# Performance work log

Measured on AMD Instinct MI355X. Metric: run time of the kernel, lower is better.

The kernel has to match this reference:

```python
import jax, jax.numpy as jnp
import numpy as np

M = 8192          # flattened tokens (batch*seq)
IN_FEATURES = 4096
OUT_FEATURES = 4096


def setup_inputs() -> dict:
    key = jax.random.key(0)
    k1, k2, k3 = jax.random.split(key, 3)
    # int8-valued activations and weights, stored as int32 (values in [-128, 127])
    x = jax.random.randint(k1, (M, IN_FEATURES), -128, 128, dtype=jnp.int32)
    int_weight = jax.random.randint(k2, (OUT_FEATURES, IN_FEATURES), -128, 127, dtype=jnp.int32)
    bias = (jax.random.normal(k3, (OUT_FEATURES,), dtype=jnp.float32) * 0.02).astype(jnp.float16)
    return {"x": x, "int_weight": int_weight, "bias": bias}


def reference(x, int_weight, bias):
    # x.to(torch.int8); quik int8Matmul: int8 GEMM with int32 accumulation, out = x @ W^T
    x_i8 = x.astype(jnp.int8)
    w_i8 = int_weight.astype(jnp.int8)
    acc = jax.lax.dot_general(
        x_i8, w_i8,
        dimension_numbers=(((1,), (1,)), ((), ())),  # [M, K] x [N, K] -> [M, N]
        preferred_element_type=jnp.int32,
    )
    # .to(torch.float16) then bias add (fused epilogue target)
    return acc.astype(jnp.float16) + bias
```

## Files before the change

kernel.cpp:

```cpp
#include <hip/hip_runtime.h>

#define MDIM 8192
#define NDIM 4096
#define KDIM 4096
#define BM 256
#define BN 128
#define BK 128

typedef int v4i __attribute__((ext_vector_type(4)));
typedef int v16i __attribute__((ext_vector_type(16)));

__device__ __forceinline__ unsigned pack4(int x, int y, int z, int w) {
    return (unsigned)(x & 0xff) | ((unsigned)(y & 0xff) << 8) |
           ((unsigned)(z & 0xff) << 16) | ((unsigned)w << 24);
}

__global__ __launch_bounds__(256) void pack_tiled(const int* __restrict__ x,
                                                  const int* __restrict__ w,
                                                  uint4* __restrict__ xp,
                                                  uint4* __restrict__ wp) {
    __shared__ unsigned lds32[256 * 33];
    const int wg  = blockIdx.x;
    const int tid = threadIdx.x;
    const int kq   = tid & 31;
    const int rsub = tid >> 5;

    if (wg < 1024) {
        const int mtile = wg >> 5, kiter = wg & 31;
        const int* base = x + (size_t)(mtile * 256) * KDIM + kiter * 128;
#pragma unroll
        for (int it = 0; it < 32; ++it) {
            const int row = it * 8 + rsub;
            int4 v = *(const int4*)(base + (size_t)row * KDIM + kq * 4);
            lds32[row * 33 + kq] = pack4(v.x, v.y, v.z, v.w);
        }
        __syncthreads();
        uint4* dst = xp + (size_t)(mtile * 32 + kiter) * 8192;
#pragma unroll
        for (int it = 0; it < 8; ++it) {
            const int g = it * 256 + tid;
            const int kb = g >> 8, row = g & 255;
            const unsigned* p = &lds32[row * 33 + kb * 4];
            uint4 o;
            o.x = p[0]; o.y = p[1]; o.z = p[2]; o.w = p[3];
            dst[g] = o;
        }
    } else {
        const int ntile = (wg - 1024) >> 5, kiter = wg & 31;
        const int* base = w + (size_t)(ntile * 128) * KDIM + kiter * 128;
#pragma unroll
        for (int it = 0; it < 16; ++it) {
            const int row = it * 8 + rsub;
            int4 v = *(const int4*)(base + (size_t)row * KDIM + kq * 4);
            lds32[row * 33 + kq] = pack4(v.x, v.y, v.z, v.w);
        }
        __syncthreads();
        uint4* dst = wp + (size_t)(ntile * 32 + kiter) * 4096;
#pragma unroll
        for (int it = 0; it < 16; ++it) {
            const int g = it * 256 + tid;
            const int kb = g >> 7, row = g & 127;
            const unsigned* p = &lds32[row * 33 + kb * 4];
            uint4 o;
            o.x = p[0]; o.y = p[1]; o.z = p[2]; o.w = p[3];
            dst[g] = o;
        }
    }
}

template <bool PACKED>
__global__ __launch_bounds__(256, 2) void gemm_i8(const char* __restrict__ Ap,
                                                  const char* __restrict__ Bp,
                                                  const int* __restrict__ A32,
                                                  const int* __restrict__ B32,
                                                  const _Float16* __restrict__ bias,
                                                  _Float16* __restrict__ out) {
    __shared__ char lds[49152];

    const int tid  = threadIdx.x;
    const int lane = tid & 63;
    const int wave = tid >> 6;
    const int bm0 = blockIdx.y * BM;
    const int bn0 = blockIdx.x * BN;

    const char* apan = Ap + (size_t)blockIdx.y * (BM * KDIM) + lane * 16;
    const char* bpan = Bp + (size_t)blockIdx.x * (BN * KDIM) + lane * 16;

    int aoffs[8], boffs[4];
    if constexpr (!PACKED) {
#pragma unroll
        for (int r = 0; r < 8; ++r) {
            const int c = r * 4 + wave;
            aoffs[r] = (bm0 + (c & 3) * 64 + lane) * KDIM + (c >> 2) * 16;
        }
#pragma unroll
        for (int r = 0; r < 4; ++r) {
            const int c = r * 4 + wave;
            boffs[r] = (bn0 + (c & 1) * 64 + lane) * KDIM + (c >> 1) * 16;
        }
    }

    const int wr  = wave >> 1;
    const int wc  = wave & 1;
    const int l31 = lane & 31;
    const int kg  = lane >> 5;
    int abase[4], bbase[2];
#pragma unroll
    for (int mt = 0; mt < 4; ++mt)
        abase[mt] = kg * 4096 + (wr * 128 + mt * 32 + l31) * 16;
#pragma unroll
    for (int nt = 0; nt < 2; ++nt)
        bbase[nt] = 32768 + kg * 2048 + (wc * 64 + nt * 32 + l31) * 16;

    v16i acc[4][2];
#pragma unroll
    for (int mt = 0; mt < 4; ++mt)
#pragma unroll
        for (int nt = 0; nt < 2; ++nt)
#pragma unroll
            for (int i = 0; i < 16; ++i) acc[mt][nt][i] = 0;

    for (int k0 = 0; k0 < KDIM; k0 += BK) {
        if constexpr (PACKED) {
#pragma unroll
            for (int r = 0; r < 8; ++r) {
                const int c = r * 4 + wave;
                __builtin_amdgcn_global_load_lds(
                    (__attribute__((address_space(1))) void*)(apan + c * 1024),
                    (__attribute__((address_space(3))) void*)(lds + c * 1024), 16, 0, 0);
            }
#pragma unroll
            for (int r = 0; r < 4; ++r) {
                const int c = r * 4 + wave;
                __builtin_amdgcn_global_load_lds(
                    (__attribute__((address_space(1))) void*)(bpan + c * 1024),
                    (__attribute__((address_space(3))) void*)(lds + 32768 + c * 1024), 16, 0, 0);
            }
            apan += BM * BK;
            bpan += BN * BK;
        } else {
#pragma unroll
            for (int r = 0; r < 8; ++r) {
                const int c = r * 4 + wave;
                const int4* s = (const int4*)(A32 + (size_t)aoffs[r]);
                int4 v0 = s[0], v1 = s[1], v2 = s[2], v3 = s[3];
                uint4 pk;
                pk.x = pack4(v0.x, v0.y, v0.z, v0.w);
                pk.y = pack4(v1.x, v1.y, v1.z, v1.w);
                pk.z = pack4(v2.x, v2.y, v2.z, v2.w);
                pk.w = pack4(v3.x, v3.y, v3.z, v3.w);
                *(uint4*)(lds + c * 1024 + lane * 16) = pk;
                aoffs[r] += BK;
            }
#pragma unroll
            for (int r = 0; r < 4; ++r) {
                const int c = r * 4 + wave;
                const int4* s = (const int4*)(B32 + (size_t)boffs[r]);
                int4 v0 = s[0], v1 = s[1], v2 = s[2], v3 = s[3];
                uint4 pk;
                pk.x = pack4(v0.x, v0.y, v0.z, v0.w);
                pk.y = pack4(v1.x, v1.y, v1.z, v1.w);
                pk.z = pack4(v2.x, v2.y, v2.z, v2.w);
                pk.w = pack4(v3.x, v3.y, v3.z, v3.w);
                *(uint4*)(lds + 32768 + c * 1024 + lane * 16) = pk;
                boffs[r] += BK;
            }
        }
        __syncthreads();

#pragma unroll
        for (int ks = 0; ks < 4; ++ks) {
            v4i af[4], bf[2];
#pragma unroll
            for (int mt = 0; mt < 4; ++mt)
                af[mt] = *(const v4i*)(lds + abase[mt] + ks * 8192);
#pragma unroll
            for (int nt = 0; nt < 2; ++nt)
                bf[nt] = *(const v4i*)(lds + bbase[nt] + ks * 4096);
#pragma unroll
            for (int mt = 0; mt < 4; ++mt)
#pragma unroll
                for (int nt = 0; nt < 2; ++nt)
                    acc[mt][nt] = __builtin_amdgcn_mfma_i32_32x32x32_i8(
                        af[mt], bf[nt], acc[mt][nt], 0, 0, 0);
        }

        __syncthreads();
    }

    const _Float16 bv0 = bias[bn0 + wc * 64 + l31];
    const _Float16 bv1 = bias[bn0 + wc * 64 + 32 + l31];
#pragma unroll
    for (int mt = 0; mt < 4; ++mt) {
#pragma unroll
        for (int nt = 0; nt < 2; ++nt) {
            const int gcol = bn0 + wc * 64 + nt * 32 + l31;
            const _Float16 bb = nt ? bv1 : bv0;
#pragma unroll
            for (int r = 0; r < 16; ++r) {
                const int rit  = (r & 3) + 8 * (r >> 2) + 4 * kg;
                const int grow = bm0 + wr * 128 + mt * 32 + rit;
                _Float16 h = (_Float16)(float)acc[mt][nt][r] + bb;
                out[(size_t)grow * NDIM + gcol] = h;
            }
        }
    }
}

extern "C" void kernel_launch(void* const* d_in, const int* in_sizes, int n_in,
                              void* d_out, int out_size, void* d_ws, size_t ws_size,
                              hipStream_t stream) {
    const int* x = (const int*)d_in[0];
    const int* w = (const int*)d_in[1];
    const _Float16* bias = (const _Float16*)d_in[2];
    _Float16* out = (_Float16*)d_out;

    const size_t xbytes = (size_t)MDIM * KDIM;
    const size_t wbytes = (size_t)NDIM * KDIM;

    if (ws_size >= xbytes + wbytes) {
        char* xp = (char*)d_ws;
        char* wp = xp + xbytes;
        pack_tiled<<<2048, 256, 0, stream>>>(x, w, (uint4*)xp, (uint4*)wp);
        gemm_i8<true><<<dim3(NDIM / BN, MDIM / BM), 256, 0, stream>>>(
            xp, wp, nullptr, nullptr, bias, out);
    } else {
        gemm_i8<false><<<dim3(NDIM / BN, MDIM / BM), 256, 0, stream>>>(
            nullptr, nullptr, x, w, bias, out);
    }
}
```

Measured before the change: 411.8 us.

## Load packed B fragments straight into registers and fix packed tile strides

Result: faster. 396.8 us (-3.6%).

```diff
diff --git a/kernel.cpp b/kernel.cpp
--- a/kernel.cpp
+++ b/kernel.cpp
@@ -35,7 +35,7 @@
             lds32[row * 33 + kq] = pack4(v.x, v.y, v.z, v.w);
         }
         __syncthreads();
-        uint4* dst = xp + (size_t)(mtile * 32 + kiter) * 8192;
+        uint4* dst = xp + (size_t)(mtile * 32 + kiter) * 2048;
 #pragma unroll
         for (int it = 0; it < 8; ++it) {
             const int g = it * 256 + tid;
@@ -55,11 +55,14 @@
             lds32[row * 33 + kq] = pack4(v.x, v.y, v.z, v.w);
         }
         __syncthreads();
-        uint4* dst = wp + (size_t)(ntile * 32 + kiter) * 4096;
-#pragma unroll
-        for (int it = 0; it < 16; ++it) {
-            const int g = it * 256 + tid;
-            const int kb = g >> 7, row = g & 127;
+        uint4* dst = wp + (size_t)(ntile * 32 + kiter) * 1024;
+#pragma unroll
+        for (int it = 0; it < 4; ++it) {
+            const int g  = it * 256 + tid;
+            const int ln = g & 63, h = g >> 6;
+            const int wc2 = h >> 3, nt = (h >> 2) & 1, ks = h & 3;
+            const int row = wc2 * 64 + nt * 32 + (ln & 31);
+            const int kb  = 2 * ks + (ln >> 5);
             const unsigned* p = &lds32[row * 33 + kb * 4];
             uint4 o;
             o.x = p[0]; o.y = p[1]; o.z = p[2]; o.w = p[3];
@@ -75,42 +78,34 @@
                                                   const int* __restrict__ B32,
                                                   const _Float16* __restrict__ bias,
                                                   _Float16* __restrict__ out) {
-    __shared__ char lds[49152];
+    __shared__ char lds[32768];
 
     const int tid  = threadIdx.x;
     const int lane = tid & 63;
     const int wave = tid >> 6;
     const int bm0 = blockIdx.y * BM;
     const int bn0 = blockIdx.x * BN;
-
-    const char* apan = Ap + (size_t)blockIdx.y * (BM * KDIM) + lane * 16;
-    const char* bpan = Bp + (size_t)blockIdx.x * (BN * KDIM) + lane * 16;
-
-    int aoffs[8], boffs[4];
-    if constexpr (!PACKED) {
-#pragma unroll
-        for (int r = 0; r < 8; ++r) {
-            const int c = r * 4 + wave;
-            aoffs[r] = (bm0 + (c & 3) * 64 + lane) * KDIM + (c >> 2) * 16;
-        }
-#pragma unroll
-        for (int r = 0; r < 4; ++r) {
-            const int c = r * 4 + wave;
-            boffs[r] = (bn0 + (c & 1) * 64 + lane) * KDIM + (c >> 1) * 16;
-        }
-    }
-
     const int wr  = wave >> 1;
     const int wc  = wave & 1;
     const int l31 = lane & 31;
     const int kg  = lane >> 5;
-    int abase[4], bbase[2];
+
+    const char* apan = Ap + (size_t)blockIdx.y * (BM * KDIM) + lane * 16;
+    const char* bpan = Bp + (size_t)blockIdx.x * (BN * KDIM) + wc * 8192 + lane * 16;
+
+    int aoffs[8];
+    if constexpr (!PACKED) {
+#pragma unroll
+        for (int r = 0; r < 8; ++r) {
+            const int c = r * 4 + wave;
+            aoffs[r] = (bm0 + (c & 3) * 64 + lane) * KDIM + (c >> 2) * 16;
+        }
+    }
+
+    int abase[4];
 #pragma unroll
     for (int mt = 0; mt < 4; ++mt)
         abase[mt] = kg * 4096 + (wr * 128 + mt * 32 + l31) * 16;
-#pragma unroll
-    for (int nt = 0; nt < 2; ++nt)
-        bbase[nt] = 32768 + kg * 2048 + (wc * 64 + nt * 32 + l31) * 16;
 
     v16i acc[4][2];
 #pragma unroll
@@ -121,6 +116,7 @@
             for (int i = 0; i < 16; ++i) acc[mt][nt][i] = 0;
 
     for (int k0 = 0; k0 < KDIM; k0 += BK) {
+        v4i bf[2][4];
         if constexpr (PACKED) {
 #pragma unroll
             for (int r = 0; r < 8; ++r) {
@@ -130,12 +126,10 @@
                     (__attribute__((address_space(3))) void*)(lds + c * 1024), 16, 0, 0);
             }
 #pragma unroll
-            for (int r = 0; r < 4; ++r) {
-                const int c = r * 4 + wave;
-                __builtin_amdgcn_global_load_lds(
-                    (__attribute__((address_space(1))) void*)(bpan + c * 1024),
-                    (__attribute__((address_space(3))) void*)(lds + 32768 + c * 1024), 16, 0, 0);
-            }
+            for (int nt = 0; nt < 2; ++nt)
+#pragma unroll
+                for (int ks = 0; ks < 4; ++ks)
+                    bf[nt][ks] = *(const v4i*)(bpan + (nt * 4 + ks) * 1024);
             apan += BM * BK;
             bpan += BN * BK;
         } else {
@@ -153,36 +147,33 @@
                 aoffs[r] += BK;
             }
 #pragma unroll
-            for (int r = 0; r < 4; ++r) {
-                const int c = r * 4 + wave;
-                const int4* s = (const int4*)(B32 + (size_t)boffs[r]);
-                int4 v0 = s[0], v1 = s[1], v2 = s[2], v3 = s[3];
-                uint4 pk;
-                pk.x = pack4(v0.x, v0.y, v0.z, v0.w);
-                pk.y = pack4(v1.x, v1.y, v1.z, v1.w);
-                pk.z = pack4(v2.x, v2.y, v2.z, v2.w);
-                pk.w = pack4(v3.x, v3.y, v3.z, v3.w);
-                *(uint4*)(lds + 32768 + c * 1024 + lane * 16) = pk;
-                boffs[r] += BK;
-            }
+            for (int nt = 0; nt < 2; ++nt)
+#pragma unroll
+                for (int ks = 0; ks < 4; ++ks) {
+                    const int* s = B32 + (size_t)(bn0 + wc * 64 + nt * 32 + l31) * KDIM
+                                   + k0 + (2 * ks + kg) * 16;
+                    int4 v0 = ((const int4*)s)[0], v1 = ((const int4*)s)[1];
+                    int4 v2 = ((const int4*)s)[2], v3 = ((const int4*)s)[3];
+                    bf[nt][ks][0] = (int)pack4(v0.x, v0.y, v0.z, v0.w);
+                    bf[nt][ks][1] = (int)pack4(v1.x, v1.y, v1.z, v1.w);
+                    bf[nt][ks][2] = (int)pack4(v2.x, v2.y, v2.z, v2.w);
+                    bf[nt][ks][3] = (int)pack4(v3.x, v3.y, v3.z, v3.w);
+                }
         }
         __syncthreads();
 
 #pragma unroll
         for (int ks = 0; ks < 4; ++ks) {
-            v4i af[4], bf[2];
+            v4i af[4];
 #pragma unroll
             for (int mt = 0; mt < 4; ++mt)
                 af[mt] = *(const v4i*)(lds + abase[mt] + ks * 8192);
 #pragma unroll
-            for (int nt = 0; nt < 2; ++nt)
-                bf[nt] = *(const v4i*)(lds + bbase[nt] + ks * 4096);
-#pragma unroll
             for (int mt = 0; mt < 4; ++mt)
 #pragma unroll
                 for (int nt = 0; nt < 2; ++nt)
                     acc[mt][nt] = __builtin_amdgcn_mfma_i32_32x32x32_i8(
-                        af[mt], bf[nt], acc[mt][nt], 0, 0, 0);
+                        af[mt], bf[nt][ks], acc[mt][nt], 0, 0, 0);
         }
 
         __syncthreads();
```
